# Kernel tuning notes

Hardware: AMD Instinct MI355X
Metric: run time of the kernel (lower is better)

## Reference

```python
import jax, jax.numpy as jnp
import numpy as np

N_HEAD = 12
N_EMBD = 768
N_EMBD_SIDE = 384
N_EMBD_KQ = 192
N_EMBD_OUT = N_EMBD + N_EMBD_SIDE  # 1152
B, L = 2, 2048


def setup_inputs() -> dict:
    key = jax.random.key(0)
    ks = jax.random.split(key, 12)
    s = 0.02
    return {
        "x": jax.random.normal(ks[0], (B, L, N_EMBD), dtype=jnp.float32),
        "side": jax.random.normal(ks[1], (B, L, N_EMBD_SIDE), dtype=jnp.float32),
        # weights stored as (in_features, out_features) so y = x @ W + b
        "Wq": jax.random.normal(ks[2], (N_EMBD_SIDE, N_EMBD_KQ), dtype=jnp.float32) * s,
        "bq": jnp.zeros((N_EMBD_KQ,), dtype=jnp.float32),
        "Wkv": jax.random.normal(ks[3], (N_EMBD_OUT, N_EMBD_KQ + N_EMBD_OUT), dtype=jnp.float32) * s,
        "bkv": jnp.zeros((N_EMBD_KQ + N_EMBD_OUT,), dtype=jnp.float32),
        "Wproj": jax.random.normal(ks[4], (N_EMBD_OUT, N_EMBD_OUT), dtype=jnp.float32) * s,
        "bproj": jnp.zeros((N_EMBD_OUT,), dtype=jnp.float32),
        "Wemb": jax.random.normal(ks[5], (N_EMBD_SIDE, N_EMBD_OUT), dtype=jnp.float32) * s,
        "bemb": jnp.zeros((N_EMBD_OUT,), dtype=jnp.float32),
    }


def reference(x, side, Wq, bq, Wkv, bkv, Wproj, bproj, Wemb, bemb):
    batch, length, _ = x.shape
    hd_kq = N_EMBD_KQ // N_HEAD   # 16
    hd_v = N_EMBD_OUT // N_HEAD   # 96

    q = (side @ Wq + bq).reshape(batch, length, N_HEAD, hd_kq).transpose(0, 2, 1, 3)  # [B,H,L,dk]
    kv = jnp.concatenate((x, side), axis=2) @ Wkv + bkv
    k = kv[:, :, :N_EMBD_KQ].reshape(batch, length, N_HEAD, hd_kq).transpose(0, 2, 1, 3)
    v = kv[:, :, N_EMBD_KQ:].reshape(batch, length, N_HEAD, hd_v).transpose(0, 2, 1, 3)

    first = (side[:, 0] @ Wemb + bemb).reshape(batch, N_HEAD, 1, hd_v)  # [B,H,1,dv]

    # shifted causal mask: row i attends to j < i; row 0 copies row 1 (attends to j==0)
    mask = jnp.tril(jnp.ones((length, length), dtype=bool), k=-1)
    mask = mask.at[0].set(mask[1])

    scale = 1.0 / jnp.sqrt(jnp.asarray(hd_kq, dtype=q.dtype))
    scores = jnp.einsum("bhqd,bhkd->bhqk", q, k) * scale
    scores = jnp.where(mask, scores, -jnp.inf)
    attn = jax.nn.softmax(scores, axis=-1)
    y = jnp.einsum("bhqk,bhkd->bhqd", attn, v)  # [B,H,L,dv]

    # special-case first token: replaced by learned embedding of side[:,0]
    y = jnp.concatenate((first, y[:, :, 1:]), axis=2)
    y = y.transpose(0, 2, 1, 3).reshape(batch, length, N_EMBD_OUT)
    return y @ Wproj + bproj
```

## Files before the change

kernel.cpp:

```cpp
#include <hip/hip_runtime.h>
#include <hip/hip_bf16.h>
#include <math.h>

#define N_HEADS 12
#define L_SEQ   2048
#define BATCH   2
#define D_KQ    192
#define D_OUT   1152
#define D_KV    1344
#define D_KVQ   1536
#define D_X     768
#define D_SIDE  384
#define HD_K    16
#define HD_V    96
#define M_ROWS  4096

typedef __attribute__((ext_vector_type(8))) short bf16x8;
typedef __attribute__((ext_vector_type(4))) float f32x4;

__device__ inline ushort f2b(float f){ __hip_bfloat16 h = __float2bfloat16(f);
                                       return *reinterpret_cast<ushort*>(&h); }

__device__ inline void gload_lds16(const ushort* g, ushort* l) {
    __builtin_amdgcn_global_load_lds(
        (const __attribute__((address_space(1))) void*)g,
        (__attribute__((address_space(3))) void*)l, 16, 0, 0);
}

#define SWZ(r, c) ((((r) * 64) + (c)) ^ (((r) & 7) << 3))

__global__ __launch_bounds__(256)
void cvt_inputs(const float* __restrict__ x, const float* __restrict__ side,
                ushort* __restrict__ xs_bf) {
    const int gid = blockIdx.x * 256 + threadIdx.x;
    if (gid < 786432) {
        const int r = gid / 192, c = (gid - r * 192) * 4;
        float4 v = *reinterpret_cast<const float4*>(&x[(size_t)r * D_X + c]);
        ushort4 o = make_ushort4(f2b(v.x), f2b(v.y), f2b(v.z), f2b(v.w));
        *reinterpret_cast<ushort4*>(&xs_bf[(size_t)r * D_OUT + c]) = o;
    } else {
        const int g2 = gid - 786432;
        const int r = g2 / 96, c = (g2 - r * 96) * 4;
        float4 v = *reinterpret_cast<const float4*>(&side[(size_t)r * D_SIDE + c]);
        ushort4 o = make_ushort4(f2b(v.x), f2b(v.y), f2b(v.z), f2b(v.w));
        *reinterpret_cast<ushort4*>(&xs_bf[(size_t)r * D_OUT + D_X + c]) = o;
    }
}

__global__ __launch_bounds__(256)
void transpose_kvq(const float* __restrict__ Wkv, const float* __restrict__ Wq,
                   ushort* __restrict__ Wt) {
    __shared__ float t[32][33];
    const int n0 = blockIdx.x * 32, k0 = blockIdx.y * 32;
    const int tx = threadIdx.x & 31, ty = threadIdx.x >> 5;
#pragma unroll
    for (int i = 0; i < 4; i++) {
        const int k = k0 + ty + i * 8, n = n0 + tx;
        float v;
        if (n < D_KV)        v = Wkv[(size_t)k * D_KV + n];
        else if (k >= D_X)   v = Wq[(size_t)(k - D_X) * D_KQ + (n - D_KV)];
        else                 v = 0.f;
        t[ty + i * 8][tx] = v;
    }
    __syncthreads();
#pragma unroll
    for (int i = 0; i < 4; i++) {
        const int n = n0 + ty + i * 8;
        Wt[(size_t)n * D_OUT + k0 + tx] = f2b(t[tx][ty + i * 8]);
    }
}

__global__ __launch_bounds__(256)
void transpose_cvt(const float* __restrict__ W, ushort* __restrict__ Wt,
                   int K, int N) {
    __shared__ float t[32][33];
    const int n0 = blockIdx.x * 32, k0 = blockIdx.y * 32;
    const int tx = threadIdx.x & 31, ty = threadIdx.x >> 5;
#pragma unroll
    for (int i = 0; i < 4; i++)
        t[ty + i * 8][tx] = W[(size_t)(k0 + ty + i * 8) * N + n0 + tx];
    __syncthreads();
#pragma unroll
    for (int i = 0; i < 4; i++) {
        const int n = n0 + ty + i * 8;
        Wt[(size_t)n * K + k0 + tx] = f2b(t[tx][ty + i * 8]);
    }
}

template<int MODE>
__global__ __launch_bounds__(256)
void gemm_mfma(const ushort* __restrict__ A, const ushort* __restrict__ Bt,
               const float* __restrict__ bias, const float* __restrict__ bias2,
               void* __restrict__ Cv, ushort* __restrict__ vt,
               ushort* __restrict__ qout, int M, int N, int K) {
    __shared__ ushort As[128 * 32];
    __shared__ ushort Bs[128 * 32];
    const int tid = threadIdx.x;
    const int w = tid >> 6, lane = tid & 63;
    const int wr = w >> 1, wc = w & 1;
    const int n0 = blockIdx.x * 128, m0 = blockIdx.y * 128;
    const int l4 = lane & 3, lrow = lane >> 2;
    const int kgrp = lane >> 4, l16 = lane & 15;

    f32x4 acc[4][4];
#pragma unroll
    for (int i = 0; i < 4; i++)
#pragma unroll
        for (int j = 0; j < 4; j++)
            acc[i][j] = (f32x4){0.f, 0.f, 0.f, 0.f};

    for (int kt = 0; kt < K; kt += 32) {
        __syncthreads();
#pragma unroll
        for (int r = 0; r < 2; r++) {
            const int seg = r * 4 + w;
            const int trow = seg * 16 + lrow;
            gload_lds16(&A [(size_t)(m0 + trow) * K + kt + l4 * 8], &As[seg * 512]);
            gload_lds16(&Bt[(size_t)(n0 + trow) * K + kt + l4 * 8], &Bs[seg * 512]);
        }
        __syncthreads();

        bf16x8 a[4], b[4];
#pragma unroll
        for (int i = 0; i < 4; i++)
            a[i] = *reinterpret_cast<const bf16x8*>(
                &As[(wr * 64 + i * 16 + l16) * 32 + kgrp * 8]);
#pragma unroll
        for (int j = 0; j < 4; j++)
            b[j] = *reinterpret_cast<const bf16x8*>(
                &Bs[(wc * 64 + j * 16 + l16) * 32 + kgrp * 8]);
#pragma unroll
        for (int i = 0; i < 4; i++)
#pragma unroll
            for (int j = 0; j < 4; j++)
                acc[i][j] = __builtin_amdgcn_mfma_f32_16x16x32_bf16(
                    a[i], b[j], acc[i][j], 0, 0, 0);
    }

    const int rgrp = lane >> 4;
#pragma unroll
    for (int j = 0; j < 4; j++) {
        const int col = n0 + wc * 64 + j * 16 + l16;
        if constexpr (MODE == 2) {
            if (col < D_KQ) {
                const float bv = bias[col];
#pragma unroll
                for (int i = 0; i < 4; i++) {
                    const int row0 = m0 + wr * 64 + i * 16 + rgrp * 4;
#pragma unroll
                    for (int rg = 0; rg < 4; rg++)
                        ((ushort*)Cv)[(size_t)(row0 + rg) * D_KQ + col] =
                            f2b(acc[i][j][rg] + bv);
                }
            } else if (col < D_KV) {
                const float bv = bias[col];
                const int hh = (col - D_KQ) / HD_V;
                const int dd = (col - D_KQ) % HD_V;
                const int bb = m0 >> 11;
                ushort* vrow = vt + ((size_t)(bb * N_HEADS + hh) * HD_V + dd) * L_SEQ
                                  + (m0 & 2047);
#pragma unroll
                for (int i = 0; i < 4; i++) {
                    const int r0 = wr * 64 + i * 16 + rgrp * 4;
                    ushort4 o = make_ushort4(
                        f2b(acc[i][j][0] + bv), f2b(acc[i][j][1] + bv),
                        f2b(acc[i][j][2] + bv), f2b(acc[i][j][3] + bv));
                    *reinterpret_cast<ushort4*>(&vrow[r0]) = o;
                }
            } else {
                const int qc = col - D_KV;
                const float bv = bias2[qc];
#pragma unroll
                for (int i = 0; i < 4; i++) {
                    const int row0 = m0 + wr * 64 + i * 16 + rgrp * 4;
#pragma unroll
                    for (int rg = 0; rg < 4; rg++)
                        qout[(size_t)(row0 + rg) * D_KQ + qc] =
                            f2b(acc[i][j][rg] + bv);
                }
            }
            continue;
        }
        if (col >= N) continue;
        const float bv = bias[col];
#pragma unroll
        for (int i = 0; i < 4; i++) {
            const int row0 = m0 + wr * 64 + i * 16 + rgrp * 4;
#pragma unroll
            for (int rg = 0; rg < 4; rg++)
                ((float*)Cv)[(size_t)(row0 + rg) * N + col] = acc[i][j][rg] + bv;
        }
    }
}

__global__ __launch_bounds__(128)
void attn_mfma(const ushort* __restrict__ qbuf, const ushort* __restrict__ kb,
               const ushort* __restrict__ vtg, ushort* __restrict__ yb) {
    __shared__ ushort Vt[96 * 64];
    __shared__ ushort Ks[64 * 16];
    __shared__ __align__(16) ushort Kz[8];
    __shared__ ushort Ps[2][16 * 64];

    const int tid = threadIdx.x;
    const int w = tid >> 6, lane = tid & 63;
    const int l16 = lane & 15, kgrp = lane >> 4;

    const int i = blockIdx.x, j5 = i & 255, g = i >> 8;
    const int tb = j5 & 63;
    const int t  = (g & 1) ? (63 - tb) : tb;
    const int hb = (g << 2) | (j5 >> 6);
    const int h = hb % N_HEADS, b = hb / N_HEADS;

    if (tid < 8) Kz[tid] = 0;

    const ushort* vt_h  = vtg + (size_t)(b * N_HEADS + h) * HD_V * L_SEQ;
    const ushort* kbase = kb + (size_t)b * L_SEQ * D_KQ;
    const int rowbase = t * 32;
    const int nt = (t >> 1) + 1;
    const int rowoff = (t & 1) * 32;

    int voff[6];
#pragma unroll
    for (int s6 = 0; s6 < 6; s6++) {
        const int L = (w * 6 + s6) * 1024 + lane * 16;
        const int X = L ^ (((L >> 7) & 7) << 4);
        voff[s6] = (X >> 7) * L_SEQ + ((X >> 1) & 63);
    }
    int koff;
    {
        const int elem = (w * 1024 + lane * 16) >> 1;
        koff = (elem >> 4) * D_KQ + h * HD_K + ((elem >> 3) & 1) * 8;
    }

    bf16x8 qf = {0, 0, 0, 0, 0, 0, 0, 0};
    if (kgrp < 2)
        qf = *reinterpret_cast<const bf16x8*>(
            qbuf + ((size_t)b * L_SEQ + rowbase + w * 16 + l16) * D_KQ
                 + h * HD_K + kgrp * 8);

    float m[4] = {-INFINITY, -INFINITY, -INFINITY, -INFINITY};
    float l[4] = {0.f, 0.f, 0.f, 0.f};
    f32x4 acc[6];
#pragma unroll
    for (int ob = 0; ob < 6; ob++) acc[ob] = (f32x4){0.f, 0.f, 0.f, 0.f};

    for (int t2 = 0; t2 < nt; t2++) {
        const int j0 = t2 * 64;
        const bool diag = (t2 == nt - 1);
        __syncthreads();

        gload_lds16(kbase + (size_t)j0 * D_KQ + koff, &Ks[w * 512]);
#pragma unroll
        for (int s6 = 0; s6 < 6; s6++)
            gload_lds16(vt_h + voff[s6] + j0, &Vt[(w * 6 + s6) * 512]);
        __syncthreads();

        __builtin_amdgcn_s_setprio(1);
        f32x4 s[4];
#pragma unroll
        for (int f = 0; f < 4; f++) {
            const ushort* kp = (kgrp < 2) ? &Ks[(f * 16 + l16) * 16 + kgrp * 8]
                                          : &Kz[0];
            bf16x8 kf = *reinterpret_cast<const bf16x8*>(kp);
            s[f] = __builtin_amdgcn_mfma_f32_16x16x32_bf16(
                qf, kf, (f32x4){0.f, 0.f, 0.f, 0.f}, 0, 0, 0);
        }
        __builtin_amdgcn_s_setprio(0);

#pragma unroll
        for (int f = 0; f < 4; f++)
#pragma unroll
            for (int r = 0; r < 4; r++) {
                float v = s[f][r] * 0.25f;
                if (diag) {
                    const int row32 = w * 16 + kgrp * 4 + r;
                    const int key64 = f * 16 + l16;
                    if (key64 >= rowoff + row32) v = -INFINITY;
                }
                s[f][r] = v;
            }

        float scl[4];
#pragma unroll
        for (int r = 0; r < 4; r++) {
            float mt = fmaxf(fmaxf(s[0][r], s[1][r]), fmaxf(s[2][r], s[3][r]));
            mt = fmaxf(mt, __shfl_xor(mt, 1));
            mt = fmaxf(mt, __shfl_xor(mt, 2));
            mt = fmaxf(mt, __shfl_xor(mt, 4));
            mt = fmaxf(mt, __shfl_xor(mt, 8));
            const float mn = fmaxf(m[r], mt);
            scl[r] = __expf(m[r] - mn);
            m[r] = mn;
            float ps = 0.f;
#pragma unroll
            for (int f = 0; f < 4; f++) {
                float p = __expf(s[f][r] - mn);
                s[f][r] = p;
                ps += p;
            }
            ps += __shfl_xor(ps, 1);
            ps += __shfl_xor(ps, 2);
            ps += __shfl_xor(ps, 4);
            ps += __shfl_xor(ps, 8);
            l[r] = l[r] * scl[r] + ps;
        }

#pragma unroll
        for (int f = 0; f < 4; f++)
#pragma unroll
            for (int r = 0; r < 4; r++)
                Ps[w][SWZ(kgrp * 4 + r, f * 16 + l16)] = f2b(s[f][r]);
#pragma unroll
        for (int ob = 0; ob < 6; ob++)
#pragma unroll
            for (int r = 0; r < 4; r++)
                acc[ob][r] *= scl[r];

        asm volatile("s_waitcnt lgkmcnt(0)" ::: "memory");
        __builtin_amdgcn_sched_barrier(0);

        bf16x8 pa0 = *reinterpret_cast<const bf16x8*>(&Ps[w][SWZ(l16, kgrp * 8)]);
        bf16x8 pa1 = *reinterpret_cast<const bf16x8*>(&Ps[w][SWZ(l16, 32 + kgrp * 8)]);
        __builtin_amdgcn_s_setprio(1);
#pragma unroll
        for (int ob = 0; ob < 6; ob++) {
            bf16x8 vb0 = *reinterpret_cast<const bf16x8*>(&Vt[SWZ(ob * 16 + l16, kgrp * 8)]);
            bf16x8 vb1 = *reinterpret_cast<const bf16x8*>(&Vt[SWZ(ob * 16 + l16, 32 + kgrp * 8)]);
            acc[ob] = __builtin_amdgcn_mfma_f32_16x16x32_bf16(pa0, vb0, acc[ob], 0, 0, 0);
            acc[ob] = __builtin_amdgcn_mfma_f32_16x16x32_bf16(pa1, vb1, acc[ob], 0, 0, 0);
        }
        __builtin_amdgcn_s_setprio(0);
    }

#pragma unroll
    for (int r = 0; r < 4; r++) {
        const float inv = 1.f / l[r];
        ushort* dst = yb + ((size_t)b * L_SEQ + rowbase + w * 16 + kgrp * 4 + r) * D_OUT
                        + h * HD_V;
#pragma unroll
        for (int ob = 0; ob < 6; ob++)
            dst[ob * 16 + l16] = f2b(acc[ob][r] * inv);
    }
}

__global__ __launch_bounds__(128)
void first_kernel(const float* __restrict__ side, const float* __restrict__ Wemb,
                  const float* __restrict__ bemb, ushort* __restrict__ yb) {
    const int o = blockIdx.x * 128 + threadIdx.x;
    const int b = blockIdx.y;
    const float* s = side + (size_t)b * L_SEQ * D_SIDE;
    float acc = bemb[o];
    for (int k = 0; k < D_SIDE; k++)
        acc += s[k] * Wemb[(size_t)k * D_OUT + o];
    yb[(size_t)b * L_SEQ * D_OUT + o] = f2b(acc);
}

extern "C" void kernel_launch(void* const* d_in, const int* in_sizes, int n_in,
                              void* d_out, int out_size, void* d_ws, size_t ws_size,
                              hipStream_t stream) {
    const float* x     = (const float*)d_in[0];
    const float* side  = (const float*)d_in[1];
    const float* Wq    = (const float*)d_in[2];
    const float* bq    = (const float*)d_in[3];
    const float* Wkv   = (const float*)d_in[4];
    const float* bkv   = (const float*)d_in[5];
    const float* Wproj = (const float*)d_in[6];
    const float* bproj = (const float*)d_in[7];
    const float* Wemb  = (const float*)d_in[8];
    const float* bemb  = (const float*)d_in[9];
    float* out = (float*)d_out;

    char* ws = (char*)d_ws;
    ushort* xs_bf   = (ushort*)(ws + 0);
    ushort* wkvq_t  = (ushort*)(ws + 9437184);
    ushort* wproj_t = (ushort*)(ws + 12976128);
    ushort* qbuf    = (ushort*)(ws + 15630336);
    ushort* kbuf    = (ushort*)(ws + 17203200);
    ushort* vtg     = (ushort*)(ws + 18776064);
    ushort* ybuf    = (ushort*)(ws + 28213248);

    cvt_inputs<<<4608, 256, 0, stream>>>(x, side, xs_bf);
    transpose_kvq<<<dim3(48, 36), 256, 0, stream>>>(Wkv, Wq, wkvq_t);
    transpose_cvt<<<dim3(36, 36), 256, 0, stream>>>(Wproj, wproj_t, D_OUT, D_OUT);

    gemm_mfma<2><<<dim3(12, 32), 256, 0, stream>>>(
        xs_bf, wkvq_t, bkv, bq, kbuf, vtg, qbuf, M_ROWS, D_KVQ, D_OUT);

    attn_mfma<<<1536, 128, 0, stream>>>(qbuf, kbuf, vtg, ybuf);

    first_kernel<<<dim3(9, BATCH), 128, 0, stream>>>(side, Wemb, bemb, ybuf);

    gemm_mfma<0><<<dim3(9, 32), 256, 0, stream>>>(
        ybuf, wproj_t, bproj, nullptr, out, nullptr, nullptr, M_ROWS, D_OUT, D_OUT);
}
```

Measured before the change: 259.0 us.

## Double-buffer GEMM LDS tiles and prefetch K/V loads in attention loop

The GEMM kernel gets double-buffered LDS tiles. The next k-tile's global-to-LDS loads are issued before computing on the current one, synchronised with explicit vmcnt waits and raw barriers. In attention, K is double-buffered and prefetched one tile ahead, and V loads are issued after QK^T so they overlap with the softmax. The goal is to hide global load latency behind MFMA work, at the cost of doubling GEMM LDS use (which may reduce occupancy) and relying on hand-tuned waitcnt counts for correctness.

```diff
diff --git a/kernel.cpp b/kernel.cpp
--- a/kernel.cpp
+++ b/kernel.cpp
@@ -93,8 +93,8 @@
                const float* __restrict__ bias, const float* __restrict__ bias2,
                void* __restrict__ Cv, ushort* __restrict__ vt,
                ushort* __restrict__ qout, int M, int N, int K) {
-    __shared__ ushort As[128 * 32];
-    __shared__ ushort Bs[128 * 32];
+    __shared__ __align__(16) ushort As[2][128 * 32];
+    __shared__ __align__(16) ushort Bs[2][128 * 32];
     const int tid = threadIdx.x;
     const int w = tid >> 6, lane = tid & 63;
     const int wr = w >> 1, wc = w & 1;
@@ -109,32 +109,52 @@
         for (int j = 0; j < 4; j++)
             acc[i][j] = (f32x4){0.f, 0.f, 0.f, 0.f};
 
-    for (int kt = 0; kt < K; kt += 32) {
-        __syncthreads();
+    auto stage = [&](int buf, int kt) {
 #pragma unroll
         for (int r = 0; r < 2; r++) {
             const int seg = r * 4 + w;
             const int trow = seg * 16 + lrow;
-            gload_lds16(&A [(size_t)(m0 + trow) * K + kt + l4 * 8], &As[seg * 512]);
-            gload_lds16(&Bt[(size_t)(n0 + trow) * K + kt + l4 * 8], &Bs[seg * 512]);
-        }
-        __syncthreads();
+            gload_lds16(&A [(size_t)(m0 + trow) * K + kt * 32 + l4 * 8],
+                        &As[buf][seg * 512]);
+            gload_lds16(&Bt[(size_t)(n0 + trow) * K + kt * 32 + l4 * 8],
+                        &Bs[buf][seg * 512]);
+        }
+    };
+
+    const int KT = K >> 5;
+    stage(0, 0);
+    int cur = 0;
+    for (int kt = 0; kt < KT; ++kt) {
+        if (kt + 1 < KT) {
+            stage(cur ^ 1, kt + 1);
+            asm volatile("s_waitcnt vmcnt(4)" ::: "memory");
+        } else {
+            asm volatile("s_waitcnt vmcnt(0)" ::: "memory");
+        }
+        __builtin_amdgcn_s_barrier();
+        __builtin_amdgcn_sched_barrier(0);
 
         bf16x8 a[4], b[4];
 #pragma unroll
         for (int i = 0; i < 4; i++)
             a[i] = *reinterpret_cast<const bf16x8*>(
-                &As[(wr * 64 + i * 16 + l16) * 32 + kgrp * 8]);
+                &As[cur][(wr * 64 + i * 16 + l16) * 32 + kgrp * 8]);
 #pragma unroll
         for (int j = 0; j < 4; j++)
             b[j] = *reinterpret_cast<const bf16x8*>(
-                &Bs[(wc * 64 + j * 16 + l16) * 32 + kgrp * 8]);
+                &Bs[cur][(wc * 64 + j * 16 + l16) * 32 + kgrp * 8]);
+        __builtin_amdgcn_s_setprio(1);
 #pragma unroll
         for (int i = 0; i < 4; i++)
 #pragma unroll
             for (int j = 0; j < 4; j++)
                 acc[i][j] = __builtin_amdgcn_mfma_f32_16x16x32_bf16(
                     a[i], b[j], acc[i][j], 0, 0, 0);
+        __builtin_amdgcn_s_setprio(0);
+
+        __builtin_amdgcn_s_barrier();
+        __builtin_amdgcn_sched_barrier(0);
+        cur ^= 1;
     }
 
     const int rgrp = lane >> 4;
@@ -196,10 +216,9 @@
 __global__ __launch_bounds__(128)
 void attn_mfma(const ushort* __restrict__ qbuf, const ushort* __restrict__ kb,
                const ushort* __restrict__ vtg, ushort* __restrict__ yb) {
-    __shared__ ushort Vt[96 * 64];
-    __shared__ ushort Ks[64 * 16];
-    __shared__ __align__(16) ushort Kz[8];
-    __shared__ ushort Ps[2][16 * 64];
+    __shared__ __align__(16) ushort Vt[96 * 64];
+    __shared__ __align__(16) ushort Ks[2][1024];
+    __shared__ __align__(16) ushort Ps[2][16 * 64];
 
     const int tid = threadIdx.x;
     const int w = tid >> 6, lane = tid & 63;
@@ -211,8 +230,6 @@
     const int hb = (g << 2) | (j5 >> 6);
     const int h = hb % N_HEADS, b = hb / N_HEADS;
 
-    if (tid < 8) Kz[tid] = 0;
-
     const ushort* vt_h  = vtg + (size_t)(b * N_HEADS + h) * HD_V * L_SEQ;
     const ushort* kbase = kb + (size_t)b * L_SEQ * D_KQ;
     const int rowbase = t * 32;
@@ -244,28 +261,36 @@
 #pragma unroll
     for (int ob = 0; ob < 6; ob++) acc[ob] = (f32x4){0.f, 0.f, 0.f, 0.f};
 
+    gload_lds16(kbase + koff, &Ks[0][w * 512]);
+    int cur = 0;
+
     for (int t2 = 0; t2 < nt; t2++) {
         const int j0 = t2 * 64;
         const bool diag = (t2 == nt - 1);
-        __syncthreads();
-
-        gload_lds16(kbase + (size_t)j0 * D_KQ + koff, &Ks[w * 512]);
+
+        asm volatile("s_waitcnt vmcnt(0) lgkmcnt(0)" ::: "memory");
+        __builtin_amdgcn_s_barrier();
+        __builtin_amdgcn_sched_barrier(0);
+
+        __builtin_amdgcn_s_setprio(1);
+        f32x4 s[4];
+#pragma unroll
+        for (int f = 0; f < 4; f++) {
+            bf16x8 kf = {0, 0, 0, 0, 0, 0, 0, 0};
+            if (kgrp < 2)
+                kf = *reinterpret_cast<const bf16x8*>(
+                    &Ks[cur][(f * 16 + l16) * 16 + kgrp * 8]);
+            s[f] = __builtin_amdgcn_mfma_f32_16x16x32_bf16(
+                qf, kf, (f32x4){0.f, 0.f, 0.f, 0.f}, 0, 0, 0);
+        }
+        __builtin_amdgcn_s_setprio(0);
+
 #pragma unroll
         for (int s6 = 0; s6 < 6; s6++)
             gload_lds16(vt_h + voff[s6] + j0, &Vt[(w * 6 + s6) * 512]);
-        __syncthreads();
-
-        __builtin_amdgcn_s_setprio(1);
-        f32x4 s[4];
-#pragma unroll
-        for (int f = 0; f < 4; f++) {
-            const ushort* kp = (kgrp < 2) ? &Ks[(f * 16 + l16) * 16 + kgrp * 8]
-                                          : &Kz[0];
-            bf16x8 kf = *reinterpret_cast<const bf16x8*>(kp);
-            s[f] = __builtin_amdgcn_mfma_f32_16x16x32_bf16(
-                qf, kf, (f32x4){0.f, 0.f, 0.f, 0.f}, 0, 0, 0);
-        }
-        __builtin_amdgcn_s_setprio(0);
+        if (t2 + 1 < nt)
+            gload_lds16(kbase + (size_t)(j0 + 64) * D_KQ + koff,
+                        &Ks[cur ^ 1][w * 512]);
 
 #pragma unroll
         for (int f = 0; f < 4; f++)
@@ -316,7 +341,12 @@
             for (int r = 0; r < 4; r++)
                 acc[ob][r] *= scl[r];
 
-        asm volatile("s_waitcnt lgkmcnt(0)" ::: "memory");
+        if (t2 + 1 < nt)
+            asm volatile("s_waitcnt vmcnt(1) lgkmcnt(0)" ::: "memory");
+        else
+            asm volatile("s_waitcnt vmcnt(0) lgkmcnt(0)" ::: "memory");
+        __builtin_amdgcn_sched_barrier(0);
+        __builtin_amdgcn_s_barrier();
         __builtin_amdgcn_sched_barrier(0);
 
         bf16x8 pa0 = *reinterpret_cast<const bf16x8*>(&Ps[w][SWZ(l16, kgrp * 8)]);
@@ -330,6 +360,7 @@
             acc[ob] = __builtin_amdgcn_mfma_f32_16x16x32_bf16(pa1, vb1, acc[ob], 0, 0, 0);
         }
         __builtin_amdgcn_s_setprio(0);
+        cur ^= 1;
     }
 
 #pragma unroll
```

After: 277.4 us. +7.1%, slower.
